# Kernel tuning notes

Hardware: AMD Instinct MI355X
Metric: run time of the kernel (lower is better)

## Reference

```python
import jax, jax.numpy as jnp
import numpy as np

LN_EPS = 1e-5

def _ln(x, g, b):
    m = x.mean(-1, keepdims=True)
    v = ((x - m) ** 2).mean(-1, keepdims=True)
    return (x - m) / jnp.sqrt(v + LN_EPS) * g + b

def _mlp(x, W1, b1, g, beta, W2, b2):
    # Linear -> LayerNorm -> ReLU -> Linear
    h = jax.nn.relu(_ln(x @ W1 + b1, g, beta))
    return h @ W2 + b2

def setup_inputs() -> dict:
    key = jax.random.key(0)
    N, E, C_in, C_out, H = 50000, 800000, 64, 64, 64
    ks = jax.random.split(key, 16)
    def rn(k, shape, fan_in):
        return jax.random.normal(k, shape, jnp.float32) * (fan_in ** -0.5)
    return dict(
        x=jax.random.normal(ks[0], (N, C_in), jnp.float32),
        pos=jax.random.normal(ks[1], (N, 3), jnp.float32),
        edge_index=jax.random.randint(ks[2], (2, E), 0, N, jnp.int32),
        W_in=rn(ks[3], (C_in, C_in), C_in), b_in=jnp.zeros((C_in,), jnp.float32),
        W_lin=rn(ks[4], (C_in, C_out), C_in),
        W_src=rn(ks[5], (C_in, C_out), C_in),
        W_dst=rn(ks[6], (C_in, C_out), C_in),
        pos_W1=rn(ks[7], (3, H), 3), pos_b1=jnp.zeros((H,), jnp.float32),
        pos_g=jnp.ones((H,), jnp.float32), pos_beta=jnp.zeros((H,), jnp.float32),
        pos_W2=rn(ks[8], (H, C_out), H), pos_b2=jnp.zeros((C_out,), jnp.float32),
        att_W1=rn(ks[9], (C_out, H), C_out), att_b1=jnp.zeros((H,), jnp.float32),
        att_g=jnp.ones((H,), jnp.float32), att_beta=jnp.zeros((H,), jnp.float32),
        att_W2=rn(ks[10], (H, C_out), H), att_b2=jnp.zeros((C_out,), jnp.float32),
        W_out=rn(ks[11], (C_out, C_out), C_out), b_out=jnp.zeros((C_out,), jnp.float32),
    )

def reference(x, pos, edge_index, W_in, b_in, W_lin, W_src, W_dst,
              pos_W1, pos_b1, pos_g, pos_beta, pos_W2, pos_b2,
              att_W1, att_b1, att_g, att_beta, att_W2, att_b2,
              W_out, b_out):
    N = x.shape[0]
    # lin_in + relu
    x = jax.nn.relu(x @ W_in + b_in)
    # PointTransformerConv with add_self_loops=True (PyG default)
    loops = jnp.arange(N, dtype=edge_index.dtype)
    src = jnp.concatenate([edge_index[0], loops])  # j (neighbors)
    dst = jnp.concatenate([edge_index[1], loops])  # i (centers)
    a_src = x @ W_src           # [N, C_out]
    a_dst = x @ W_dst           # [N, C_out]
    v = x @ W_lin               # [N, C_out]
    # per-edge positional encoding delta = pos_nn(pos_i - pos_j)
    delta = _mlp(pos[dst] - pos[src], pos_W1, pos_b1, pos_g, pos_beta, pos_W2, pos_b2)  # [E, C_out]
    alpha = _mlp(a_dst[dst] - a_src[src] + delta, att_W1, att_b1, att_g, att_beta, att_W2, att_b2)
    # per-destination, per-channel softmax over variable-size neighborhoods
    amax = jax.ops.segment_max(alpha, dst, num_segments=N)
    e = jnp.exp(alpha - amax[dst])
    denom = jax.ops.segment_sum(e, dst, num_segments=N)
    w = e / jnp.clip(denom[dst], 1e-16)
    # weighted scatter-sum of (value_j + delta)
    out = jax.ops.segment_sum(w * (v[src] + delta), dst, num_segments=N)  # [N, C_out]
    # lin_out + relu
    return jax.nn.relu(out @ W_out + b_out)
```

## Files before the change

kernel.cpp:

```cpp
#include <hip/hip_runtime.h>
#include <hip/hip_bf16.h>


typedef __bf16 bf16x8 __attribute__((ext_vector_type(8)));
typedef short  s16x8  __attribute__((ext_vector_type(8)));
typedef float  f32x4  __attribute__((ext_vector_type(4)));

#define SWZ(b) ((b) ^ ((((b) >> 7) & 7) << 4))

__device__ __forceinline__ unsigned short f2b(float f) {
  union { __hip_bfloat16 h; unsigned short u; } c;
  c.h = __float2bfloat16(f);
  return c.u;
}
__device__ __forceinline__ unsigned int pack2(float a, float b) {
  return (unsigned int)f2b(a) | ((unsigned int)f2b(b) << 16);
}
__device__ __forceinline__ void lds_fence() {
  asm volatile("s_waitcnt lgkmcnt(0)" ::: "memory");
  __builtin_amdgcn_sched_barrier(0);
}

__device__ __forceinline__ void stage_wt(const float* __restrict__ W, char* dst, int tid) {
  for (int idx = tid; idx < 2048; idx += 256) {
    int c  = idx >> 5;
    int k2 = (idx & 31) << 1;
    float v0 = W[k2 * 64 + c];
    float v1 = W[(k2 + 1) * 64 + c];
    int byte = c * 128 + k2 * 2;
    *(unsigned int*)(dst + SWZ(byte)) = pack2(v0, v1);
  }
}

__device__ __forceinline__ void gemm16(const char* actb, const char* wb,
                                       int g, int m, f32x4 acc[4]) {
  #pragma unroll
  for (int kk = 0; kk < 2; kk++) {
    s16x8 af = *(const s16x8*)(actb + SWZ(m * 128 + g * 16 + kk * 64));
    #pragma unroll
    for (int t = 0; t < 4; t++) {
      s16x8 bf = *(const s16x8*)(wb + SWZ((t * 16 + m) * 128 + g * 16 + kk * 64));
      acc[t] = __builtin_amdgcn_mfma_f32_16x16x32_bf16(
          __builtin_bit_cast(bf16x8, af), __builtin_bit_cast(bf16x8, bf), acc[t], 0, 0, 0);
    }
  }
}

__global__ __launch_bounds__(256, 3) void node_mfma_kernel(
    const float* __restrict__ x,
    const float* __restrict__ W_in, const float* __restrict__ b_in,
    const float* __restrict__ W_lin, const float* __restrict__ W_src, const float* __restrict__ W_dst,
    float* __restrict__ a_src, float* __restrict__ a_dst, float* __restrict__ vv,
    int N)
{
  __shared__ __align__(16) char sWinT[8192], sWsT[8192], sWdT[8192], sWlT[8192], sX[8192];
  __shared__ float sB[64];
  int tid = threadIdx.x;
  stage_wt(W_in,  sWinT, tid);
  stage_wt(W_src, sWsT,  tid);
  stage_wt(W_dst, sWdT,  tid);
  stage_wt(W_lin, sWlT,  tid);
  if (tid < 64) sB[tid] = b_in[tid];

  const int lane = tid & 63, wv = tid >> 6;
  const int g = lane >> 4, m = lane & 15;
  const int ew = wv << 4;
  const int srow = tid >> 2, sc0 = (tid & 3) << 4;
  const int ntile = (N + 63) >> 6;

  for (int tile = blockIdx.x; tile < ntile; tile += gridDim.x) {
    const int rbase = tile << 6;
    __syncthreads();
    {
      int gr = rbase + srow; if (gr >= N) gr = N - 1;
      const float4* src = (const float4*)&x[(size_t)gr * 64 + sc0];
      #pragma unroll
      for (int q = 0; q < 4; q++) {
        float4 f = src[q];
        int byte = srow * 128 + sc0 * 2 + q * 8;
        *(unsigned int*)(sX + SWZ(byte))     = pack2(f.x, f.y);
        *(unsigned int*)(sX + SWZ(byte + 4)) = pack2(f.z, f.w);
      }
    }
    __syncthreads();

    f32x4 a0[4] = {};
    gemm16(sX + ew * 128, sWinT, g, m, a0);
    float x1[4][4];
    #pragma unroll
    for (int t = 0; t < 4; t++)
      #pragma unroll
      for (int r = 0; r < 4; r++) x1[t][r] = fmaxf(a0[t][r] + sB[t * 16 + m], 0.f);
    __syncthreads();
    #pragma unroll
    for (int t = 0; t < 4; t++)
      #pragma unroll
      for (int r = 0; r < 4; r++)
        *(unsigned short*)(sX + SWZ((ew + 4 * g + r) * 128 + (t * 16 + m) * 2)) = f2b(x1[t][r]);
    __syncthreads();

    f32x4 as[4] = {}, ad[4] = {}, al[4] = {};
    gemm16(sX + ew * 128, sWsT, g, m, as);
    gemm16(sX + ew * 128, sWdT, g, m, ad);
    gemm16(sX + ew * 128, sWlT, g, m, al);
    #pragma unroll
    for (int t = 0; t < 4; t++)
      #pragma unroll
      for (int r = 0; r < 4; r++) {
        int gr = rbase + ew + 4 * g + r;
        if (gr < N) {
          size_t o = (size_t)gr * 64 + t * 16 + m;
          a_src[o] = as[t][r]; a_dst[o] = ad[t][r]; vv[o] = al[t][r];
        }
      }
  }
}

__global__ void hist_kernel(const int* __restrict__ ei, int* __restrict__ deg, int E, int Etot) {
  int stride = gridDim.x * blockDim.x;
  for (int e = blockIdx.x * blockDim.x + threadIdx.x; e < Etot; e += stride) {
    int d = (e < E) ? ei[E + e] : (e - E);
    atomicAdd(&deg[d], 1);
  }
}

__global__ __launch_bounds__(256) void scanA_kernel(const int* __restrict__ deg, int* __restrict__ chunkSum, int N) {
  __shared__ int s[256];
  int i = blockIdx.x * 256 + threadIdx.x;
  s[threadIdx.x] = (i < N) ? deg[i] : 0;
  __syncthreads();
  for (int off = 128; off > 0; off >>= 1) {
    if (threadIdx.x < off) s[threadIdx.x] += s[threadIdx.x + off];
    __syncthreads();
  }
  if (threadIdx.x == 0) chunkSum[blockIdx.x] = s[0];
}

__global__ __launch_bounds__(256) void scanB_kernel(const int* __restrict__ chunkSum, int* __restrict__ chunkPre, int nchunk) {
  __shared__ int s[256];
  int t = threadIdx.x;
  int v = (t < nchunk) ? chunkSum[t] : 0;
  s[t] = v; __syncthreads();
  for (int off = 1; off < 256; off <<= 1) {
    int x = (t >= off) ? s[t - off] : 0;
    __syncthreads();
    s[t] += x;
    __syncthreads();
  }
  if (t < nchunk) chunkPre[t] = s[t] - v;
}

__global__ __launch_bounds__(256) void scanC_kernel(const int* __restrict__ deg, const int* __restrict__ chunkPre,
                                                    int* __restrict__ cursor, int N) {
  __shared__ int s[256];
  int t = threadIdx.x;
  int i = blockIdx.x * 256 + t;
  int v = (i < N) ? deg[i] : 0;
  s[t] = v; __syncthreads();
  for (int off = 1; off < 256; off <<= 1) {
    int x = (t >= off) ? s[t - off] : 0;
    __syncthreads();
    s[t] += x;
    __syncthreads();
  }
  if (i < N) cursor[i] = chunkPre[blockIdx.x] + s[t] - v;
}

__global__ void scatter_kernel(const int* __restrict__ ei, int* __restrict__ cursor,
                               const float* __restrict__ pos,
                               int* __restrict__ srcS, int* __restrict__ dstS,
                               float4* __restrict__ pd4,
                               int E, int Etot) {
  int stride = gridDim.x * blockDim.x;
  for (int e = blockIdx.x * blockDim.x + threadIdx.x; e < Etot; e += stride) {
    int s, d;
    if (e < E) { s = ei[e]; d = ei[E + e]; }
    else       { s = e - E; d = s; }
    int p = atomicAdd(&cursor[d], 1);
    srcS[p] = s; dstS[p] = d;
    float4 q;
    q.x = pos[d * 3 + 0] - pos[s * 3 + 0];
    q.y = pos[d * 3 + 1] - pos[s * 3 + 1];
    q.z = pos[d * 3 + 2] - pos[s * 3 + 2];
    q.w = 0.f;
    pd4[p] = q;
  }
}

__global__ __launch_bounds__(256, 3) void edge_kernel(
    const int* __restrict__ srcS, const int* __restrict__ dstS, const float4* __restrict__ pd4,
    const float* __restrict__ a_src_g, const float* __restrict__ a_dst_g, const float* __restrict__ v_g,
    const float* __restrict__ pos_W1, const float* __restrict__ pos_b1,
    const float* __restrict__ pos_gg, const float* __restrict__ pos_beta,
    const float* __restrict__ pos_W2, const float* __restrict__ pos_b2,
    const float* __restrict__ att_W1, const float* __restrict__ att_b1,
    const float* __restrict__ att_gg, const float* __restrict__ att_beta,
    const float* __restrict__ att_W2, const float* __restrict__ att_b2,
    float* __restrict__ numer, float* __restrict__ denom,
    int G, int gpw)
{
  __shared__ __align__(16) char sW2t[8192], sA1t[8192], sA2t[8192];
  __shared__ __align__(16) char sAct[4][2048];
  __shared__ float sAcc[4][4][128];
  __shared__ float sPW1[192];
  __shared__ float sPB1[64], sPG[64], sPBeta[64], sPB2[64];
  __shared__ float sAB1[64], sAG[64], sABeta[64], sAB2[64];

  int tid = threadIdx.x;
  stage_wt(pos_W2, sW2t, tid);
  stage_wt(att_W1, sA1t, tid);
  stage_wt(att_W2, sA2t, tid);
  for (int i = tid; i < 192; i += 256) sPW1[i] = pos_W1[i];
  if (tid < 64) {
    sPB1[tid] = pos_b1[tid]; sPG[tid] = pos_gg[tid]; sPBeta[tid] = pos_beta[tid]; sPB2[tid] = pos_b2[tid];
    sAB1[tid] = att_b1[tid]; sAG[tid] = att_gg[tid]; sABeta[tid] = att_beta[tid]; sAB2[tid] = att_b2[tid];
  }
  for (int i = tid; i < 4 * 4 * 128; i += 256) ((float*)sAcc)[i] = 0.f;
  __syncthreads();

  const int lane = tid & 63, wv = tid >> 6;
  const int g = lane >> 4, m = lane & 15;
  char* myAct = sAct[wv];
  float (*myAcc)[128] = sAcc[wv];

  const int w  = blockIdx.x * 4 + wv;
  const int g0 = w * gpw;
  int g1 = g0 + gpw; if (g1 > G) g1 = G;

  for (int grp = g0; grp < g1; ++grp) {
    const int ebase = grp << 4;

    float4 pdr[4];
    #pragma unroll
    for (int r = 0; r < 4; r++) pdr[r] = pd4[ebase + 4 * g + r];
    int dall[16];
    #pragma unroll
    for (int i = 0; i < 16; i++) dall[i] = dstS[ebase + i];
    int mys[4];
    #pragma unroll
    for (int r = 0; r < 4; r++) mys[r] = srcS[ebase + 4 * g + r];

    int myd[4] = {-1, -1, -1, -1};
    int sid_my[4] = {0, 0, 0, 0};
    int fd0 = dall[0], fd1 = -1, fd2 = -1, fd3 = -1;
    int cur = 0;
    #pragma unroll
    for (int i = 0; i < 16; i++) {
      if (i > 0) {
        bool b = (dall[i] != dall[i - 1]);
        cur += b ? 1 : 0;
        fd1 = (b && cur == 1) ? dall[i] : fd1;
        fd2 = (b && cur == 2) ? dall[i] : fd2;
        fd3 = (b && cur == 3) ? dall[i] : fd3;
      }
      bool mine = ((i >> 2) == g);
      const int rr = i & 3;
      if (rr == 0) { myd[0] = mine ? dall[i] : myd[0]; sid_my[0] = mine ? cur : sid_my[0]; }
      if (rr == 1) { myd[1] = mine ? dall[i] : myd[1]; sid_my[1] = mine ? cur : sid_my[1]; }
      if (rr == 2) { myd[2] = mine ? dall[i] : myd[2]; sid_my[2] = mine ? cur : sid_my[2]; }
      if (rr == 3) { myd[3] = mine ? dall[i] : myd[3]; sid_my[3] = mine ? cur : sid_my[3]; }
    }
    const int ns = cur + 1;

    float adst[16], asrc[16];
    #pragma unroll
    for (int r = 0; r < 4; r++) {
      int dm = myd[r] < 0 ? 0 : myd[r];
      int sm = mys[r];
      #pragma unroll
      for (int t = 0; t < 4; t++) {
        adst[r * 4 + t] = a_dst_g[(size_t)dm * 64 + t * 16 + m];
        asrc[r * 4 + t] = a_src_g[(size_t)sm * 64 + t * 16 + m];
      }
    }

    {
      float h[4][4];
      #pragma unroll
      for (int r = 0; r < 4; r++) {
        float p0 = pdr[r].x, p1 = pdr[r].y, p2 = pdr[r].z;
        #pragma unroll
        for (int t = 0; t < 4; t++) {
          int c = t * 16 + m;
          h[t][r] = fmaf(p0, sPW1[c], fmaf(p1, sPW1[64 + c], fmaf(p2, sPW1[128 + c], sPB1[c])));
        }
      }
      #pragma unroll
      for (int r = 0; r < 4; r++) {
        float s = h[0][r] + h[1][r] + h[2][r] + h[3][r];
        s += __shfl_xor(s, 1); s += __shfl_xor(s, 2); s += __shfl_xor(s, 4); s += __shfl_xor(s, 8);
        float mean = s * (1.f / 64.f);
        float q = 0.f;
        #pragma unroll
        for (int t = 0; t < 4; t++) { float dd = h[t][r] - mean; q = fmaf(dd, dd, q); }
        q += __shfl_xor(q, 1); q += __shfl_xor(q, 2); q += __shfl_xor(q, 4); q += __shfl_xor(q, 8);
        float rs = rsqrtf(q * (1.f / 64.f) + 1e-5f);
        #pragma unroll
        for (int t = 0; t < 4; t++) {
          int c = t * 16 + m;
          float val = fmaxf(fmaf((h[t][r] - mean) * rs, sPG[c], sPBeta[c]), 0.f);
          *(unsigned short*)(myAct + SWZ((4 * g + r) * 128 + c * 2)) = f2b(val);
        }
      }
    }
    lds_fence();

    f32x4 dacc[4] = {};
    gemm16(myAct, sW2t, g, m, dacc);
    float del[4][4];
    #pragma unroll
    for (int t = 0; t < 4; t++)
      #pragma unroll
      for (int r = 0; r < 4; r++) del[t][r] = dacc[t][r] + sPB2[t * 16 + m];
    lds_fence();

    float vv[16];
    #pragma unroll
    for (int r = 0; r < 4; r++)
      #pragma unroll
      for (int t = 0; t < 4; t++)
        vv[r * 4 + t] = v_g[(size_t)mys[r] * 64 + t * 16 + m];

    #pragma unroll
    for (int r = 0; r < 4; r++)
      #pragma unroll
      for (int t = 0; t < 4; t++) {
        float a = adst[r * 4 + t] - asrc[r * 4 + t] + del[t][r];
        *(unsigned short*)(myAct + SWZ((4 * g + r) * 128 + (t * 16 + m) * 2)) = f2b(a);
      }
    lds_fence();

    f32x4 acc2[4] = {};
    gemm16(myAct, sA1t, g, m, acc2);
    float h2[4][4];
    #pragma unroll
    for (int t = 0; t < 4; t++)
      #pragma unroll
      for (int r = 0; r < 4; r++) h2[t][r] = acc2[t][r] + sAB1[t * 16 + m];
    #pragma unroll
    for (int r = 0; r < 4; r++) {
      float s = h2[0][r] + h2[1][r] + h2[2][r] + h2[3][r];
      s += __shfl_xor(s, 1); s += __shfl_xor(s, 2); s += __shfl_xor(s, 4); s += __shfl_xor(s, 8);
      float mean = s * (1.f / 64.f);
      float q = 0.f;
      #pragma unroll
      for (int t = 0; t < 4; t++) { float dd = h2[t][r] - mean; q = fmaf(dd, dd, q); }
      q += __shfl_xor(q, 1); q += __shfl_xor(q, 2); q += __shfl_xor(q, 4); q += __shfl_xor(q, 8);
      float rs = rsqrtf(q * (1.f / 64.f) + 1e-5f);
      #pragma unroll
      for (int t = 0; t < 4; t++) {
        int c = t * 16 + m;
        h2[t][r] = fmaxf(fmaf((h2[t][r] - mean) * rs, sAG[c], sABeta[c]), 0.f);
      }
    }
    lds_fence();
    #pragma unroll
    for (int t = 0; t < 4; t++)
      #pragma unroll
      for (int r = 0; r < 4; r++)
        *(unsigned short*)(myAct + SWZ((4 * g + r) * 128 + (t * 16 + m) * 2)) = f2b(h2[t][r]);
    lds_fence();

    f32x4 acc3[4] = {};
    gemm16(myAct, sA2t, g, m, acc3);

    {
      float aN[4] = {0.f, 0.f, 0.f, 0.f}, aD[4] = {0.f, 0.f, 0.f, 0.f};
      int curS = -1, curD = 0;
      #pragma unroll
      for (int r = 0; r < 4; r++) {
        int d = myd[r];
        if (d < 0) continue;
        int sgid = sid_my[r];
        if (sgid != curS) {
          if (curS >= 0) {
            if (curS < 4) {
              #pragma unroll
              for (int t = 0; t < 4; t++) {
                atomicAdd(&myAcc[curS][t * 16 + m], aN[t]);
                atomicAdd(&myAcc[curS][64 + t * 16 + m], aD[t]);
              }
            } else {
              #pragma unroll
              for (int t = 0; t < 4; t++) {
                atomicAdd(&numer[(size_t)curD * 64 + t * 16 + m], aN[t]);
                atomicAdd(&denom[(size_t)curD * 64 + t * 16 + m], aD[t]);
              }
            }
          }
          curS = sgid; curD = d;
          #pragma unroll
          for (int t = 0; t < 4; t++) { aN[t] = 0.f; aD[t] = 0.f; }
        }
        #pragma unroll
        for (int t = 0; t < 4; t++) {
          float ee = __expf(acc3[t][r] + sAB2[t * 16 + m]);
          aN[t] = fmaf(ee, vv[r * 4 + t] + del[t][r], aN[t]);
          aD[t] += ee;
        }
      }
      if (curS >= 0) {
        if (curS < 4) {
          #pragma unroll
          for (int t = 0; t < 4; t++) {
            atomicAdd(&myAcc[curS][t * 16 + m], aN[t]);
            atomicAdd(&myAcc[curS][64 + t * 16 + m], aD[t]);
          }
        } else {
          #pragma unroll
          for (int t = 0; t < 4; t++) {
            atomicAdd(&numer[(size_t)curD * 64 + t * 16 + m], aN[t]);
            atomicAdd(&denom[(size_t)curD * 64 + t * 16 + m], aD[t]);
          }
        }
      }
    }
    lds_fence();

    {
      const int nsc = ns < 4 ? ns : 4;
      const int fdk[1] = {0}; (void)fdk;
      #pragma unroll
      for (int k = 0; k < 4; k++) {
        int dd = (k == 0) ? fd0 : (k == 1) ? fd1 : (k == 2) ? fd2 : fd3;
        if (k < nsc && dd >= 0) {
          float nv = myAcc[k][lane];
          float dv = myAcc[k][64 + lane];
          atomicAdd(&numer[(size_t)dd * 64 + lane], nv);
          atomicAdd(&denom[(size_t)dd * 64 + lane], dv);
          myAcc[k][lane] = 0.f;
          myAcc[k][64 + lane] = 0.f;
        }
      }
    }
    lds_fence();
  }
}

__global__ __launch_bounds__(256) void out_mfma_kernel(
    const float* __restrict__ numer, const float* __restrict__ denom,
    const float* __restrict__ W_out, const float* __restrict__ b_out,
    float* __restrict__ out, int N)
{
  __shared__ __align__(16) char sWoT[8192], sX[8192];
  __shared__ float sB[64];
  int tid = threadIdx.x;
  stage_wt(W_out, sWoT, tid);
  if (tid < 64) sB[tid] = b_out[tid];

  const int lane = tid & 63, wv = tid >> 6;
  const int g = lane >> 4, m = lane & 15;
  const int ew = wv << 4;
  const int srow = tid >> 2, sc0 = (tid & 3) << 4;
  const int ntile = (N + 63) >> 6;

  for (int tile = blockIdx.x; tile < ntile; tile += gridDim.x) {
    const int rbase = tile << 6;
    __syncthreads();
    {
      int gr = rbase + srow; if (gr >= N) gr = N - 1;
      const float4* nsrc = (const float4*)&numer[(size_t)gr * 64 + sc0];
      const float4* dsrc = (const float4*)&denom[(size_t)gr * 64 + sc0];
      #pragma unroll
      for (int q = 0; q < 4; q++) {
        float4 fn = nsrc[q], fd = dsrc[q];
        float m0 = fn.x / fmaxf(fd.x, 1e-16f);
        float m1 = fn.y / fmaxf(fd.y, 1e-16f);
        float m2 = fn.z / fmaxf(fd.z, 1e-16f);
        float m3 = fn.w / fmaxf(fd.w, 1e-16f);
        int byte = srow * 128 + sc0 * 2 + q * 8;
        *(unsigned int*)(sX + SWZ(byte))     = pack2(m0, m1);
        *(unsigned int*)(sX + SWZ(byte + 4)) = pack2(m2, m3);
      }
    }
    __syncthreads();
    f32x4 acc[4] = {};
    gemm16(sX + ew * 128, sWoT, g, m, acc);
    #pragma unroll
    for (int t = 0; t < 4; t++)
      #pragma unroll
      for (int r = 0; r < 4; r++) {
        int gr = rbase + ew + 4 * g + r;
        if (gr < N) out[(size_t)gr * 64 + t * 16 + m] = fmaxf(acc[t][r] + sB[t * 16 + m], 0.f);
      }
  }
}

extern "C" void kernel_launch(void* const* d_in, const int* in_sizes, int n_in,
                              void* d_out, int out_size, void* d_ws, size_t ws_size,
                              hipStream_t stream) {
  (void)n_in; (void)out_size; (void)ws_size;
  const float* x        = (const float*)d_in[0];
  const float* pos      = (const float*)d_in[1];
  const int*   ei       = (const int*)  d_in[2];
  const float* W_in     = (const float*)d_in[3];
  const float* b_in     = (const float*)d_in[4];
  const float* W_lin    = (const float*)d_in[5];
  const float* W_src    = (const float*)d_in[6];
  const float* W_dst    = (const float*)d_in[7];
  const float* pos_W1   = (const float*)d_in[8];
  const float* pos_b1   = (const float*)d_in[9];
  const float* pos_g    = (const float*)d_in[10];
  const float* pos_beta = (const float*)d_in[11];
  const float* pos_W2   = (const float*)d_in[12];
  const float* pos_b2   = (const float*)d_in[13];
  const float* att_W1   = (const float*)d_in[14];
  const float* att_b1   = (const float*)d_in[15];
  const float* att_g    = (const float*)d_in[16];
  const float* att_beta = (const float*)d_in[17];
  const float* att_W2   = (const float*)d_in[18];
  const float* att_b2   = (const float*)d_in[19];
  const float* W_out    = (const float*)d_in[20];
  const float* b_out    = (const float*)d_in[21];

  const int N    = in_sizes[0] / 64;
  const int E    = in_sizes[2] / 2;
  const int Etot = E + N;
  const int Epad = (Etot + 15) & ~15;
  const size_t N64 = (size_t)N * 64;

  float* a_src = (float*)d_ws;
  float* a_dst = a_src + N64;
  float* v     = a_dst + N64;
  float* numer = v + N64;
  float* denom = numer + N64;
  int* deg      = (int*)(denom + N64);
  int* cursor   = deg + N;
  int* chunkSum = cursor + N;
  int* chunkPre = chunkSum + 256;
  int* srcS     = chunkPre + 256;
  int* dstS     = srcS + Epad;
  float4* pd4   = (float4*)(dstS + Epad);

  const int nchunk = (N + 255) / 256;

  hipMemsetAsync(deg, 0, (size_t)N * sizeof(int), stream);
  hipMemsetAsync(numer, 0, 2 * N64 * sizeof(float), stream);
  if (Epad > Etot) {
    hipMemsetAsync(dstS + Etot, 0xFF, (size_t)(Epad - Etot) * sizeof(int), stream);
    hipMemsetAsync(srcS + Etot, 0, (size_t)(Epad - Etot) * sizeof(int), stream);
    hipMemsetAsync(pd4 + Etot, 0, (size_t)(Epad - Etot) * sizeof(float4), stream);
  }

  hist_kernel<<<1024, 256, 0, stream>>>(ei, deg, E, Etot);
  scanA_kernel<<<nchunk, 256, 0, stream>>>(deg, chunkSum, N);
  scanB_kernel<<<1, 256, 0, stream>>>(chunkSum, chunkPre, nchunk);
  scanC_kernel<<<nchunk, 256, 0, stream>>>(deg, chunkPre, cursor, N);
  scatter_kernel<<<1024, 256, 0, stream>>>(ei, cursor, pos, srcS, dstS, pd4, E, Etot);

  const int ntileN = (N + 63) / 64;
  const int nblkN  = ntileN < 768 ? ntileN : 768;
  node_mfma_kernel<<<nblkN, 256, 0, stream>>>(x, W_in, b_in, W_lin, W_src, W_dst,
                                              a_src, a_dst, v, N);

  const int G   = Epad / 16;
  const int NB  = 768;
  const int gpw = (G + NB * 4 - 1) / (NB * 4);
  edge_kernel<<<NB, 256, 0, stream>>>(srcS, dstS, pd4, a_src, a_dst, v,
      pos_W1, pos_b1, pos_g, pos_beta, pos_W2, pos_b2,
      att_W1, att_b1, att_g, att_beta, att_W2, att_b2,
      numer, denom, G, gpw);

  out_mfma_kernel<<<nblkN, 256, 0, stream>>>(numer, denom, W_out, b_out, (float*)d_out, N);
}
```

Measured before the change: 482.2 us.

## Store node features in bf16, permute edge channels, prefetch gathers, shuffle-based segment reduction

The node kernel now writes a_src, a_dst and v as bf16, halving the bytes gathered per edge. The edge kernel stages its weights with a channel permutation so each lane owns 4 contiguous channels, which allows vectorized 8-byte gathers. The next group's indices and gathers are prefetched so they overlap with the current group's MLP math. The LDS accumulator plus second atomic pass is replaced by a wave-shuffle segmented reduction followed by direct global atomics. This trades some precision in the gathered features and adds more complex reduction logic.

```diff
diff --git a/kernel.cpp b/kernel.cpp
--- a/kernel.cpp
+++ b/kernel.cpp
@@ -16,19 +16,43 @@
 __device__ __forceinline__ unsigned int pack2(float a, float b) {
   return (unsigned int)f2b(a) | ((unsigned int)f2b(b) << 16);
 }
+__device__ __forceinline__ void unpack2(unsigned int u, float& a, float& b) {
+  union { unsigned int x; float f; } t0, t1;
+  t0.x = u << 16; t1.x = u & 0xffff0000u;
+  a = t0.f; b = t1.f;
+}
 __device__ __forceinline__ void lds_fence() {
   asm volatile("s_waitcnt lgkmcnt(0)" ::: "memory");
   __builtin_amdgcn_sched_barrier(0);
 }
+__device__ __forceinline__ f32x4 psel(bool p, f32x4 a) {
+  f32x4 z = {0.f, 0.f, 0.f, 0.f};
+  return p ? a : z;
+}
+template <int D>
+__device__ __forceinline__ f32x4 shup4(f32x4 v) {
+  f32x4 r;
+  #pragma unroll
+  for (int c = 0; c < 4; c++) r[c] = __shfl_up(v[c], D);
+  return r;
+}
+
+__device__ __forceinline__ int sigp(int p) { return 4 * (p & 15) + (p >> 4); }
 
 __device__ __forceinline__ void stage_wt(const float* __restrict__ W, char* dst, int tid) {
   for (int idx = tid; idx < 2048; idx += 256) {
     int c  = idx >> 5;
     int k2 = (idx & 31) << 1;
-    float v0 = W[k2 * 64 + c];
-    float v1 = W[(k2 + 1) * 64 + c];
-    int byte = c * 128 + k2 * 2;
-    *(unsigned int*)(dst + SWZ(byte)) = pack2(v0, v1);
+    *(unsigned int*)(dst + SWZ(c * 128 + k2 * 2)) = pack2(W[k2 * 64 + c], W[(k2 + 1) * 64 + c]);
+  }
+}
+__device__ __forceinline__ void stage_wt_sig(const float* __restrict__ W, char* dst, int tid) {
+  for (int idx = tid; idx < 2048; idx += 256) {
+    int q  = idx >> 5;
+    int p2 = (idx & 31) << 1;
+    int co = sigp(q);
+    *(unsigned int*)(dst + SWZ(q * 128 + p2 * 2)) =
+        pack2(W[sigp(p2) * 64 + co], W[sigp(p2 + 1) * 64 + co]);
   }
 }
 
@@ -50,11 +74,11 @@
     const float* __restrict__ x,
     const float* __restrict__ W_in, const float* __restrict__ b_in,
     const float* __restrict__ W_lin, const float* __restrict__ W_src, const float* __restrict__ W_dst,
-    float* __restrict__ a_src, float* __restrict__ a_dst, float* __restrict__ vv,
-    int N)
+    unsigned short* __restrict__ a_srcB, unsigned short* __restrict__ a_dstB,
+    unsigned short* __restrict__ vB, int N)
 {
   __shared__ __align__(16) char sWinT[8192], sWsT[8192], sWdT[8192], sWlT[8192], sX[8192];
-  __shared__ float sB[64];
+  __shared__ __align__(16) float sB[64];
   int tid = threadIdx.x;
   stage_wt(W_in,  sWinT, tid);
   stage_wt(W_src, sWsT,  tid);
@@ -110,7 +134,7 @@
         int gr = rbase + ew + 4 * g + r;
         if (gr < N) {
           size_t o = (size_t)gr * 64 + t * 16 + m;
-          a_src[o] = as[t][r]; a_dst[o] = ad[t][r]; vv[o] = al[t][r];
+          a_srcB[o] = f2b(as[t][r]); a_dstB[o] = f2b(ad[t][r]); vB[o] = f2b(al[t][r]);
         }
       }
   }
@@ -187,9 +211,42 @@
   }
 }
 
+struct Meta { int md[4]; int ms[4]; f32x4 pd[4]; };
+struct Gath { uint2 ad[4]; uint2 as[4]; uint2 vv[4]; };
+
+__device__ __forceinline__ Meta load_meta(const int* __restrict__ dstS, const int* __restrict__ srcS,
+                                          const float4* __restrict__ pd4, int ebase, int g) {
+  Meta M;
+  int4 a = *(const int4*)&dstS[ebase + 4 * g];
+  int4 b = *(const int4*)&srcS[ebase + 4 * g];
+  M.md[0] = a.x; M.md[1] = a.y; M.md[2] = a.z; M.md[3] = a.w;
+  M.ms[0] = b.x; M.ms[1] = b.y; M.ms[2] = b.z; M.ms[3] = b.w;
+  #pragma unroll
+  for (int r = 0; r < 4; r++) {
+    float4 p = pd4[ebase + 4 * g + r];
+    M.pd[r][0] = p.x; M.pd[r][1] = p.y; M.pd[r][2] = p.z; M.pd[r][3] = 0.f;
+  }
+  return M;
+}
+__device__ __forceinline__ Gath load_gath(const Meta& M,
+                                          const unsigned short* __restrict__ aD,
+                                          const unsigned short* __restrict__ aS,
+                                          const unsigned short* __restrict__ vB, int m) {
+  Gath G;
+  #pragma unroll
+  for (int r = 0; r < 4; r++) {
+    int dm = M.md[r] < 0 ? 0 : M.md[r];
+    G.ad[r] = *(const uint2*)&aD[(size_t)dm * 64 + 4 * m];
+    G.as[r] = *(const uint2*)&aS[(size_t)M.ms[r] * 64 + 4 * m];
+    G.vv[r] = *(const uint2*)&vB[(size_t)M.ms[r] * 64 + 4 * m];
+  }
+  return G;
+}
+
 __global__ __launch_bounds__(256, 3) void edge_kernel(
     const int* __restrict__ srcS, const int* __restrict__ dstS, const float4* __restrict__ pd4,
-    const float* __restrict__ a_src_g, const float* __restrict__ a_dst_g, const float* __restrict__ v_g,
+    const unsigned short* __restrict__ a_srcB, const unsigned short* __restrict__ a_dstB,
+    const unsigned short* __restrict__ vBg,
     const float* __restrict__ pos_W1, const float* __restrict__ pos_b1,
     const float* __restrict__ pos_gg, const float* __restrict__ pos_beta,
     const float* __restrict__ pos_W2, const float* __restrict__ pos_b2,
@@ -201,142 +258,96 @@
 {
   __shared__ __align__(16) char sW2t[8192], sA1t[8192], sA2t[8192];
   __shared__ __align__(16) char sAct[4][2048];
-  __shared__ float sAcc[4][4][128];
-  __shared__ float sPW1[192];
-  __shared__ float sPB1[64], sPG[64], sPBeta[64], sPB2[64];
-  __shared__ float sAB1[64], sAG[64], sABeta[64], sAB2[64];
+  __shared__ __align__(16) float sPW1[192];
+  __shared__ __align__(16) float sPB1[64], sPG[64], sPBeta[64], sPB2[64];
+  __shared__ __align__(16) float sAB1[64], sAG[64], sABeta[64], sAB2[64];
 
   int tid = threadIdx.x;
-  stage_wt(pos_W2, sW2t, tid);
-  stage_wt(att_W1, sA1t, tid);
-  stage_wt(att_W2, sA2t, tid);
+  stage_wt_sig(pos_W2, sW2t, tid);
+  stage_wt_sig(att_W1, sA1t, tid);
+  stage_wt_sig(att_W2, sA2t, tid);
   for (int i = tid; i < 192; i += 256) sPW1[i] = pos_W1[i];
   if (tid < 64) {
     sPB1[tid] = pos_b1[tid]; sPG[tid] = pos_gg[tid]; sPBeta[tid] = pos_beta[tid]; sPB2[tid] = pos_b2[tid];
     sAB1[tid] = att_b1[tid]; sAG[tid] = att_gg[tid]; sABeta[tid] = att_beta[tid]; sAB2[tid] = att_b2[tid];
   }
-  for (int i = tid; i < 4 * 4 * 128; i += 256) ((float*)sAcc)[i] = 0.f;
   __syncthreads();
 
   const int lane = tid & 63, wv = tid >> 6;
   const int g = lane >> 4, m = lane & 15;
   char* myAct = sAct[wv];
-  float (*myAcc)[128] = sAcc[wv];
 
   const int w  = blockIdx.x * 4 + wv;
   const int g0 = w * gpw;
   int g1 = g0 + gpw; if (g1 > G) g1 = G;
+  if (g0 >= g1) return;
+
+  const f32x4 pw0 = *(const f32x4*)&sPW1[4 * m];
+  const f32x4 pw1 = *(const f32x4*)&sPW1[64 + 4 * m];
+  const f32x4 pw2 = *(const f32x4*)&sPW1[128 + 4 * m];
+  const f32x4 pb1 = *(const f32x4*)&sPB1[4 * m];
+  const f32x4 pgv = *(const f32x4*)&sPG[4 * m];
+  const f32x4 pbv = *(const f32x4*)&sPBeta[4 * m];
+  const f32x4 pb2 = *(const f32x4*)&sPB2[4 * m];
+  const f32x4 ab1 = *(const f32x4*)&sAB1[4 * m];
+  const f32x4 agv = *(const f32x4*)&sAG[4 * m];
+  const f32x4 abv = *(const f32x4*)&sABeta[4 * m];
+  const f32x4 ab2 = *(const f32x4*)&sAB2[4 * m];
+
+  Meta Mc = load_meta(dstS, srcS, pd4, g0 << 4, g);
+  Gath Gc = load_gath(Mc, a_dstB, a_srcB, vBg, m);
 
   for (int grp = g0; grp < g1; ++grp) {
-    const int ebase = grp << 4;
-
-    float4 pdr[4];
-    #pragma unroll
-    for (int r = 0; r < 4; r++) pdr[r] = pd4[ebase + 4 * g + r];
-    int dall[16];
-    #pragma unroll
-    for (int i = 0; i < 16; i++) dall[i] = dstS[ebase + i];
-    int mys[4];
-    #pragma unroll
-    for (int r = 0; r < 4; r++) mys[r] = srcS[ebase + 4 * g + r];
-
-    int myd[4] = {-1, -1, -1, -1};
-    int sid_my[4] = {0, 0, 0, 0};
-    int fd0 = dall[0], fd1 = -1, fd2 = -1, fd3 = -1;
-    int cur = 0;
-    #pragma unroll
-    for (int i = 0; i < 16; i++) {
-      if (i > 0) {
-        bool b = (dall[i] != dall[i - 1]);
-        cur += b ? 1 : 0;
-        fd1 = (b && cur == 1) ? dall[i] : fd1;
-        fd2 = (b && cur == 2) ? dall[i] : fd2;
-        fd3 = (b && cur == 3) ? dall[i] : fd3;
-      }
-      bool mine = ((i >> 2) == g);
-      const int rr = i & 3;
-      if (rr == 0) { myd[0] = mine ? dall[i] : myd[0]; sid_my[0] = mine ? cur : sid_my[0]; }
-      if (rr == 1) { myd[1] = mine ? dall[i] : myd[1]; sid_my[1] = mine ? cur : sid_my[1]; }
-      if (rr == 2) { myd[2] = mine ? dall[i] : myd[2]; sid_my[2] = mine ? cur : sid_my[2]; }
-      if (rr == 3) { myd[3] = mine ? dall[i] : myd[3]; sid_my[3] = mine ? cur : sid_my[3]; }
-    }
-    const int ns = cur + 1;
-
-    float adst[16], asrc[16];
+    const int gnext = (grp + 1 < g1) ? grp + 1 : grp;
+    Meta Mn = load_meta(dstS, srcS, pd4, gnext << 4, g);
+
+    f32x4 hA[4];
     #pragma unroll
     for (int r = 0; r < 4; r++) {
-      int dm = myd[r] < 0 ? 0 : myd[r];
-      int sm = mys[r];
-      #pragma unroll
-      for (int t = 0; t < 4; t++) {
-        adst[r * 4 + t] = a_dst_g[(size_t)dm * 64 + t * 16 + m];
-        asrc[r * 4 + t] = a_src_g[(size_t)sm * 64 + t * 16 + m];
-      }
-    }
-
-    {
-      float h[4][4];
-      #pragma unroll
-      for (int r = 0; r < 4; r++) {
-        float p0 = pdr[r].x, p1 = pdr[r].y, p2 = pdr[r].z;
-        #pragma unroll
-        for (int t = 0; t < 4; t++) {
-          int c = t * 16 + m;
-          h[t][r] = fmaf(p0, sPW1[c], fmaf(p1, sPW1[64 + c], fmaf(p2, sPW1[128 + c], sPB1[c])));
-        }
-      }
-      #pragma unroll
-      for (int r = 0; r < 4; r++) {
-        float s = h[0][r] + h[1][r] + h[2][r] + h[3][r];
-        s += __shfl_xor(s, 1); s += __shfl_xor(s, 2); s += __shfl_xor(s, 4); s += __shfl_xor(s, 8);
-        float mean = s * (1.f / 64.f);
-        float q = 0.f;
-        #pragma unroll
-        for (int t = 0; t < 4; t++) { float dd = h[t][r] - mean; q = fmaf(dd, dd, q); }
-        q += __shfl_xor(q, 1); q += __shfl_xor(q, 2); q += __shfl_xor(q, 4); q += __shfl_xor(q, 8);
-        float rs = rsqrtf(q * (1.f / 64.f) + 1e-5f);
-        #pragma unroll
-        for (int t = 0; t < 4; t++) {
-          int c = t * 16 + m;
-          float val = fmaxf(fmaf((h[t][r] - mean) * rs, sPG[c], sPBeta[c]), 0.f);
-          *(unsigned short*)(myAct + SWZ((4 * g + r) * 128 + c * 2)) = f2b(val);
-        }
-      }
-    }
+      f32x4 h = pb1 + pw0 * Mc.pd[r][0] + pw1 * Mc.pd[r][1] + pw2 * Mc.pd[r][2];
+      float s = h[0] + h[1] + h[2] + h[3];
+      s += __shfl_xor(s, 1); s += __shfl_xor(s, 2); s += __shfl_xor(s, 4); s += __shfl_xor(s, 8);
+      float mean = s * (1.f / 64.f);
+      f32x4 dv = h - mean;
+      float q = dv[0]*dv[0] + dv[1]*dv[1] + dv[2]*dv[2] + dv[3]*dv[3];
+      q += __shfl_xor(q, 1); q += __shfl_xor(q, 2); q += __shfl_xor(q, 4); q += __shfl_xor(q, 8);
+      float rs = rsqrtf(q * (1.f / 64.f) + 1e-5f);
+      f32x4 o = dv * rs * pgv + pbv;
+      #pragma unroll
+      for (int c = 0; c < 4; c++) o[c] = fmaxf(o[c], 0.f);
+      hA[r] = o;
+    }
+    #pragma unroll
+    for (int r = 0; r < 4; r++)
+      #pragma unroll
+      for (int t = 0; t < 4; t++)
+        *(unsigned short*)(myAct + SWZ((4 * g + r) * 128 + 32 * t + 2 * m)) = f2b(hA[r][t]);
     lds_fence();
 
     f32x4 dacc[4] = {};
     gemm16(myAct, sW2t, g, m, dacc);
-    float del[4][4];
-    #pragma unroll
-    for (int t = 0; t < 4; t++)
-      #pragma unroll
-      for (int r = 0; r < 4; r++) del[t][r] = dacc[t][r] + sPB2[t * 16 + m];
-    lds_fence();
-
-    float vv[16];
-    #pragma unroll
-    for (int r = 0; r < 4; r++)
-      #pragma unroll
-      for (int t = 0; t < 4; t++)
-        vv[r * 4 + t] = v_g[(size_t)mys[r] * 64 + t * 16 + m];
-
-    #pragma unroll
-    for (int r = 0; r < 4; r++)
+    f32x4 del[4];
+    #pragma unroll
+    for (int t = 0; t < 4; t++) del[t] = dacc[t] + pb2[t];
+
+    #pragma unroll
+    for (int r = 0; r < 4; r++) {
+      float da[4], sa[4];
+      unpack2(Gc.ad[r].x, da[0], da[1]); unpack2(Gc.ad[r].y, da[2], da[3]);
+      unpack2(Gc.as[r].x, sa[0], sa[1]); unpack2(Gc.as[r].y, sa[2], sa[3]);
       #pragma unroll
       for (int t = 0; t < 4; t++) {
-        float a = adst[r * 4 + t] - asrc[r * 4 + t] + del[t][r];
-        *(unsigned short*)(myAct + SWZ((4 * g + r) * 128 + (t * 16 + m) * 2)) = f2b(a);
-      }
+        float av = da[t] - sa[t] + del[t][r];
+        *(unsigned short*)(myAct + SWZ((4 * g + r) * 128 + 32 * t + 2 * m)) = f2b(av);
+      }
+    }
     lds_fence();
 
     f32x4 acc2[4] = {};
     gemm16(myAct, sA1t, g, m, acc2);
-    float h2[4][4];
-    #pragma unroll
-    for (int t = 0; t < 4; t++)
-      #pragma unroll
-      for (int r = 0; r < 4; r++) h2[t][r] = acc2[t][r] + sAB1[t * 16 + m];
+    f32x4 h2[4];
+    #pragma unroll
+    for (int t = 0; t < 4; t++) h2[t] = acc2[t] + ab1[t];
     #pragma unroll
     for (int r = 0; r < 4; r++) {
       float s = h2[0][r] + h2[1][r] + h2[2][r] + h2[3][r];
@@ -348,92 +359,77 @@
       q += __shfl_xor(q, 1); q += __shfl_xor(q, 2); q += __shfl_xor(q, 4); q += __shfl_xor(q, 8);
       float rs = rsqrtf(q * (1.f / 64.f) + 1e-5f);
       #pragma unroll
-      for (int t = 0; t < 4; t++) {
-        int c = t * 16 + m;
-        h2[t][r] = fmaxf(fmaf((h2[t][r] - mean) * rs, sAG[c], sABeta[c]), 0.f);
-      }
-    }
-    lds_fence();
-    #pragma unroll
-    for (int t = 0; t < 4; t++)
-      #pragma unroll
-      for (int r = 0; r < 4; r++)
-        *(unsigned short*)(myAct + SWZ((4 * g + r) * 128 + (t * 16 + m) * 2)) = f2b(h2[t][r]);
+      for (int t = 0; t < 4; t++)
+        h2[t][r] = fmaxf(fmaf((h2[t][r] - mean) * rs, agv[t], abv[t]), 0.f);
+    }
+    #pragma unroll
+    for (int r = 0; r < 4; r++)
+      #pragma unroll
+      for (int t = 0; t < 4; t++)
+        *(unsigned short*)(myAct + SWZ((4 * g + r) * 128 + 32 * t + 2 * m)) = f2b(h2[t][r]);
     lds_fence();
 
     f32x4 acc3[4] = {};
     gemm16(myAct, sA2t, g, m, acc3);
 
+    Gath Gn = load_gath(Mn, a_dstB, a_srcB, vBg, m);
+
+    f32x4 nV[4], dV[4];
+    #pragma unroll
+    for (int r = 0; r < 4; r++) {
+      float vf[4];
+      unpack2(Gc.vv[r].x, vf[0], vf[1]); unpack2(Gc.vv[r].y, vf[2], vf[3]);
+      bool val = Mc.md[r] >= 0;
+      #pragma unroll
+      for (int t = 0; t < 4; t++) {
+        float e = __expf(acc3[t][r] + ab2[t]);
+        e = val ? e : 0.f;
+        nV[r][t] = e * (vf[t] + del[t][r]);
+        dV[r][t] = e;
+      }
+    }
+
     {
-      float aN[4] = {0.f, 0.f, 0.f, 0.f}, aD[4] = {0.f, 0.f, 0.f, 0.f};
-      int curS = -1, curD = 0;
+      int d3 = Mc.md[3];
+      bool s2 = (Mc.md[2] == d3);
+      bool s1 = s2 && (Mc.md[1] == d3);
+      bool s0 = s1 && (Mc.md[0] == d3);
+      f32x4 PN = nV[3] + psel(s2, nV[2]) + psel(s1, nV[1]) + psel(s0, nV[0]);
+      f32x4 PD = dV[3] + psel(s2, dV[2]) + psel(s1, dV[1]) + psel(s0, dV[0]);
+
+      int dPrev3 = __shfl_up(d3, 16);
+      int dNext0 = __shfl_down(Mc.md[0], 16);
+      bool ok1 = (g > 0) && (Mc.md[0] == dPrev3);
+      int okf = (ok1 && s0) ? 1 : 0;
+      int okf1 = __shfl_up(okf, 16);
+      int okf2 = __shfl_up(okf, 32);
+      bool ok2 = ok1 && (okf1 != 0);
+      bool ok3 = ok2 && (okf2 != 0);
+      f32x4 sh16N = shup4<16>(PN), sh32N = shup4<32>(PN), sh48N = shup4<48>(PN);
+      f32x4 sh16D = shup4<16>(PD), sh32D = shup4<32>(PD), sh48D = shup4<48>(PD);
+      f32x4 CN = psel(ok1, sh16N) + psel(ok2, sh32N) + psel(ok3, sh48N);
+      f32x4 CD = psel(ok1, sh16D) + psel(ok2, sh32D) + psel(ok3, sh48D);
+
+      int dn[4] = { Mc.md[1], Mc.md[2], Mc.md[3], (g == 3) ? (int)0x80000000 : dNext0 };
+
+      f32x4 aN = CN, aD = CD;
       #pragma unroll
       for (int r = 0; r < 4; r++) {
-        int d = myd[r];
-        if (d < 0) continue;
-        int sgid = sid_my[r];
-        if (sgid != curS) {
-          if (curS >= 0) {
-            if (curS < 4) {
-              #pragma unroll
-              for (int t = 0; t < 4; t++) {
-                atomicAdd(&myAcc[curS][t * 16 + m], aN[t]);
-                atomicAdd(&myAcc[curS][64 + t * 16 + m], aD[t]);
-              }
-            } else {
-              #pragma unroll
-              for (int t = 0; t < 4; t++) {
-                atomicAdd(&numer[(size_t)curD * 64 + t * 16 + m], aN[t]);
-                atomicAdd(&denom[(size_t)curD * 64 + t * 16 + m], aD[t]);
-              }
-            }
+        aN += nV[r]; aD += dV[r];
+        if (Mc.md[r] != dn[r]) {
+          if (Mc.md[r] >= 0) {
+            float* np = &numer[(size_t)Mc.md[r] * 64 + 4 * m];
+            float* dp = &denom[(size_t)Mc.md[r] * 64 + 4 * m];
+            #pragma unroll
+            for (int t = 0; t < 4; t++) { atomicAdd(np + t, aN[t]); atomicAdd(dp + t, aD[t]); }
           }
-          curS = sgid; curD = d;
-          #pragma unroll
-          for (int t = 0; t < 4; t++) { aN[t] = 0.f; aD[t] = 0.f; }
+          f32x4 z = {0.f, 0.f, 0.f, 0.f};
+          aN = z; aD = z;
         }
-        #pragma unroll
-        for (int t = 0; t < 4; t++) {
-          float ee = __expf(acc3[t][r] + sAB2[t * 16 + m]);
-          aN[t] = fmaf(ee, vv[r * 4 + t] + del[t][r], aN[t]);
-          aD[t] += ee;
-        }
-      }
-      if (curS >= 0) {
-        if (curS < 4) {
-          #pragma unroll
-          for (int t = 0; t < 4; t++) {
-            atomicAdd(&myAcc[curS][t * 16 + m], aN[t]);
-            atomicAdd(&myAcc[curS][64 + t * 16 + m], aD[t]);
-          }
-        } else {
-          #pragma unroll
-          for (int t = 0; t < 4; t++) {
-            atomicAdd(&numer[(size_t)curD * 64 + t * 16 + m], aN[t]);
-            atomicAdd(&denom[(size_t)curD * 64 + t * 16 + m], aD[t]);
-          }
-        }
-      }
-    }
-    lds_fence();
-
-    {
-      const int nsc = ns < 4 ? ns : 4;
-      const int fdk[1] = {0}; (void)fdk;
-      #pragma unroll
-      for (int k = 0; k < 4; k++) {
-        int dd = (k == 0) ? fd0 : (k == 1) ? fd1 : (k == 2) ? fd2 : fd3;
-        if (k < nsc && dd >= 0) {
-          float nv = myAcc[k][lane];
-          float dv = myAcc[k][64 + lane];
-          atomicAdd(&numer[(size_t)dd * 64 + lane], nv);
-          atomicAdd(&denom[(size_t)dd * 64 + lane], dv);
-          myAcc[k][lane] = 0.f;
-          myAcc[k][64 + lane] = 0.f;
-        }
-      }
-    }
-    lds_fence();
+      }
+    }
+
+    Mc = Mn; Gc = Gn;
   }
 }
 
@@ -519,18 +515,18 @@
   const int Epad = (Etot + 15) & ~15;
   const size_t N64 = (size_t)N * 64;
 
-  float* a_src = (float*)d_ws;
-  float* a_dst = a_src + N64;
-  float* v     = a_dst + N64;
-  float* numer = v + N64;
+  float* numer = (float*)d_ws;
   float* denom = numer + N64;
-  int* deg      = (int*)(denom + N64);
+  unsigned short* aSb = (unsigned short*)(denom + N64);
+  unsigned short* aDb = aSb + N64;
+  unsigned short* vBb = aDb + N64;
+  float4* pd4 = (float4*)(vBb + N64);
+  int* srcS     = (int*)(pd4 + Epad);
+  int* dstS     = srcS + Epad;
+  int* deg      = dstS + Epad;
   int* cursor   = deg + N;
   int* chunkSum = cursor + N;
   int* chunkPre = chunkSum + 256;
-  int* srcS     = chunkPre + 256;
-  int* dstS     = srcS + Epad;
-  float4* pd4   = (float4*)(dstS + Epad);
 
   const int nchunk = (N + 255) / 256;
 
@@ -551,12 +547,12 @@
   const int ntileN = (N + 63) / 64;
   const int nblkN  = ntileN < 768 ? ntileN : 768;
   node_mfma_kernel<<<nblkN, 256, 0, stream>>>(x, W_in, b_in, W_lin, W_src, W_dst,
-                                              a_src, a_dst, v, N);
+                                              aSb, aDb, vBb, N);
 
   const int G   = Epad / 16;
   const int NB  = 768;
   const int gpw = (G + NB * 4 - 1) / (NB * 4);
-  edge_kernel<<<NB, 256, 0, stream>>>(srcS, dstS, pd4, a_src, a_dst, v,
+  edge_kernel<<<NB, 256, 0, stream>>>(srcS, dstS, pd4, aSb, aDb, vBb,
       pos_W1, pos_b1, pos_g, pos_beta, pos_W2, pos_b2,
       att_W1, att_b1, att_g, att_beta, att_W2, att_b2,
       numer, denom, G, gpw);
```

Measured after the change: 431.1 us (median of 2 runs). 10.6% less time.
